# Kernel optimization log

Measured on AMD Instinct MI355X. Metric: run time of the kernel, lower is better.

The kernel has to match this reference:

```python
import jax, jax.numpy as jnp
import numpy as np

N_NODES = 100000
N_EDGES = 1600000
FEAT = 128
HID = 128
CLS = 4


def setup_inputs() -> dict:
    key = jax.random.key(0)
    ks = jax.random.split(key, 10)
    x = jax.random.normal(ks[0], (N_NODES, FEAT), dtype=jnp.float32)
    edge_index = jax.random.randint(ks[1], (2, N_EDGES), 0, N_NODES, dtype=jnp.int64)
    s1 = 1.0 / np.sqrt(FEAT)
    s2 = 1.0 / np.sqrt(HID)
    s3 = 1.0 / np.sqrt(CLS)
    return {
        "x": x,
        "edge_index": edge_index,
        "W1l": jax.random.uniform(ks[2], (HID, FEAT), jnp.float32, -s1, s1),
        "b1": jax.random.uniform(ks[3], (HID,), jnp.float32, -s1, s1),
        "W1r": jax.random.uniform(ks[4], (HID, FEAT), jnp.float32, -s1, s1),
        "W2l": jax.random.uniform(ks[5], (CLS, HID), jnp.float32, -s2, s2),
        "b2": jax.random.uniform(ks[6], (CLS,), jnp.float32, -s2, s2),
        "W2r": jax.random.uniform(ks[7], (CLS, HID), jnp.float32, -s2, s2),
        "Wlin": jax.random.uniform(ks[8], (2, CLS), jnp.float32, -s3, s3),
        "blin": jax.random.uniform(ks[9], (2,), jnp.float32, -s3, s3),
    }


def _sage_conv(h, src, dst, Wl, bl, Wr, n_nodes):
    # PyG SAGEConv (mean aggr, root_weight=True): lin_l(mean_j h_j) + lin_r(h_i)
    msg = h[src]  # [E, d] irregular gather
    agg = jax.ops.segment_sum(msg, dst, num_segments=n_nodes)  # [N, d]
    deg = jax.ops.segment_sum(jnp.ones((src.shape[0], 1), h.dtype), dst,
                              num_segments=n_nodes)  # [N, 1]
    agg = agg / jnp.maximum(deg, 1.0)
    return agg @ Wl.T + bl + h @ Wr.T


def reference(x, edge_index, W1l, b1, W1r, W2l, b2, W2r, Wlin, blin):
    n = x.shape[0]
    src, dst = edge_index[0], edge_index[1]
    h = jax.nn.relu(_sage_conv(x, src, dst, W1l, b1, W1r, n))
    # dropout is identity in eval mode (training=False)
    h = _sage_conv(h, src, dst, W2l, b2, W2r, n)  # [N, 4]
    return h @ Wlin.T + blin  # [N, 2]
```

## Files before the change

### kernel.cpp

```cpp
#include <hip/hip_runtime.h>

#define NN 100000
#define NE 1600000
#define NBUK 1563
#define EB 8192

typedef __attribute__((ext_vector_type(8))) short v8s;
typedef __attribute__((ext_vector_type(4))) float v4f;

__device__ __forceinline__ unsigned short f2bf(float f) {
  unsigned int u = __float_as_uint(f);
  unsigned int r = (u + 0x7FFFu + ((u >> 16) & 1u)) >> 16;
  return (unsigned short)r;
}
__device__ __forceinline__ float bflo(unsigned int w) { return __uint_as_float(w << 16); }
__device__ __forceinline__ float bfhi(unsigned int w) { return __uint_as_float(w & 0xFFFF0000u); }
__device__ __forceinline__ float bf2f(unsigned short w) {
  return __uint_as_float((unsigned int)w << 16);
}


__global__ void k_zerob(int* __restrict__ hist) {
  int i = blockIdx.x * blockDim.x + threadIdx.x;
  if (i < NBUK) hist[i] = 0;
}

__global__ __launch_bounds__(256) void k_hist(const int* __restrict__ dst,
                                              int* __restrict__ hist) {
  __shared__ int lh[NBUK];
  int t = threadIdx.x;
  for (int i = t; i < NBUK; i += 256) lh[i] = 0;
  __syncthreads();
  int base = blockIdx.x * 16384;
  int lim = min(16384, NE - base);
  for (int j = t; j < lim; j += 256) atomicAdd(&lh[dst[base + j] >> 6], 1);
  __syncthreads();
  for (int i = t; i < NBUK; i += 256) {
    int c = lh[i];
    if (c) atomicAdd(&hist[i], c);
  }
}

__global__ __launch_bounds__(256) void k_scanb(const int* __restrict__ hist,
                                               int* __restrict__ bbase,
                                               int* __restrict__ gcur) {
  __shared__ int sc[256];
  __shared__ int carry;
  int t = threadIdx.x;
  if (t == 0) carry = 0;
  __syncthreads();
  for (int c = 0; c < (NBUK + 255) / 256; ++c) {
    int i = c * 256 + t;
    int vv = (i < NBUK) ? hist[i] : 0;
    sc[t] = vv;
    __syncthreads();
    for (int o = 1; o < 256; o <<= 1) {
      int uu = (t >= o) ? sc[t - o] : 0;
      __syncthreads();
      sc[t] += uu;
      __syncthreads();
    }
    int excl = carry + sc[t] - vv;
    if (i < NBUK) { bbase[i] = excl; gcur[i] = excl; }
    __syncthreads();
    if (t == 0) carry += sc[255];
    __syncthreads();
  }
}

extern __shared__ char smem_dyn[];
__global__ __launch_bounds__(256) void k_scatter(const int* __restrict__ src,
                                                 const int* __restrict__ dst,
                                                 int* __restrict__ gcur,
                                                 unsigned int* __restrict__ staged) {
  unsigned int* stageP = (unsigned int*)smem_dyn;
  unsigned short* stageB = (unsigned short*)(stageP + EB);
  int* lhist  = (int*)(stageB + EB);
  int* lbase  = lhist + NBUK;
  int* lcur   = lbase + NBUK;
  int* gclaim = lcur + NBUK;
  __shared__ int sc[256];
  __shared__ int carry;
  int t = threadIdx.x;
  int e0 = blockIdx.x * EB;
  int ecnt = min(EB, NE - e0);
  for (int i = t; i < NBUK; i += 256) lhist[i] = 0;
  if (t == 0) carry = 0;
  __syncthreads();
  for (int j = t; j < ecnt; j += 256) atomicAdd(&lhist[dst[e0 + j] >> 6], 1);
  __syncthreads();
  for (int c = 0; c < (NBUK + 255) / 256; ++c) {
    int i = c * 256 + t;
    int vv = (i < NBUK) ? lhist[i] : 0;
    sc[t] = vv;
    __syncthreads();
    for (int o = 1; o < 256; o <<= 1) {
      int uu = (t >= o) ? sc[t - o] : 0;
      __syncthreads();
      sc[t] += uu;
      __syncthreads();
    }
    int excl = carry + sc[t] - vv;
    if (i < NBUK) { lbase[i] = excl; lcur[i] = excl; }
    __syncthreads();
    if (t == 0) carry += sc[255];
    __syncthreads();
  }
  for (int b = t; b < NBUK; b += 256) {
    int c = lhist[b];
    gclaim[b] = c ? atomicAdd(&gcur[b], c) : 0;
  }
  __syncthreads();
  for (int j = t; j < ecnt; j += 256) {
    int s = src[e0 + j], d = dst[e0 + j];
    int b = d >> 6;
    int lp = atomicAdd(&lcur[b], 1);
    stageP[lp] = ((unsigned int)s << 6) | (unsigned int)(d & 63);
    stageB[lp] = (unsigned short)b;
  }
  __syncthreads();
  for (int i = t; i < ecnt; i += 256) {
    int b = stageB[i];
    staged[gclaim[b] + (i - lbase[b])] = stageP[i];
  }
}

__global__ __launch_bounds__(256) void k_sort2(const unsigned int* __restrict__ staged,
                                               const int* __restrict__ bbase,
                                               const int* __restrict__ hist,
                                               int* __restrict__ csr,
                                               int* __restrict__ off,
                                               int* __restrict__ deg) {
  __shared__ int h64[64], c64[64];
  int bkt = blockIdx.x, t = threadIdx.x;
  if (t < 64) h64[t] = 0;
  __syncthreads();
  int st = bbase[bkt], cnt = hist[bkt];
  for (int j = t; j < cnt; j += 256) atomicAdd(&h64[staged[st + j] & 63], 1);
  __syncthreads();
  if (t < 64) {
    int v = h64[t];
    int inc = v;
    for (int o = 1; o < 64; o <<= 1) {
      int uu = __shfl_up(inc, o, 64);
      if (t >= o) inc += uu;
    }
    int excl = inc - v;
    c64[t] = excl;
    int node = bkt * 64 + t;
    if (node < NN) { off[node] = st + excl; deg[node] = v; }
  }
  __syncthreads();
  for (int j = t; j < cnt; j += 256) {
    unsigned pk = staged[st + j];
    int lp = atomicAdd(&c64[pk & 63], 1);
    csr[st + lp] = (int)(pk >> 6);
  }
}


__global__ void k_packw(const float* __restrict__ W1l, const float* __restrict__ W1r,
                        unsigned short* __restrict__ Wcat) {
  int i = blockIdx.x * blockDim.x + threadIdx.x;
  float f = (i < 16384) ? W1l[i] : W1r[i - 16384];
  Wcat[i] = f2bf(f);
}

__global__ __launch_bounds__(256) void k_gemm1(
    const float* __restrict__ x, const unsigned short* __restrict__ Wcat,
    unsigned short* __restrict__ u, unsigned short* __restrict__ v) {
  char* wlds = smem_dyn;
  int t = threadIdx.x;
  {
    int rsub = t >> 4, chunk = t & 15;
#pragma unroll
    for (int rd = 0; rd < 16; ++rd) {
      int row = rd * 16 + rsub;
      uint4 w4 = *(const uint4*)(Wcat + (size_t)row * 128 + chunk * 8);
      *(uint4*)(wlds + row * 272 + chunk * 16) = w4;
    }
  }

  int wave = t >> 6, l = t & 63;
  int m0 = blockIdx.x * 64 + wave * 16;
  int lr = l & 15, kq = l >> 4;
  int rowc = min(m0 + lr, NN - 1);

  v8s a[4];
#pragma unroll
  for (int ks = 0; ks < 4; ++ks) {
    const float* xp = x + (size_t)rowc * 128 + ks * 32 + kq * 8;
    float4 f0 = *(const float4*)xp;
    float4 f1 = *(const float4*)(xp + 4);
    v8s tv;
    tv[0] = (short)f2bf(f0.x); tv[1] = (short)f2bf(f0.y);
    tv[2] = (short)f2bf(f0.z); tv[3] = (short)f2bf(f0.w);
    tv[4] = (short)f2bf(f1.x); tv[5] = (short)f2bf(f1.y);
    tv[6] = (short)f2bf(f1.z); tv[7] = (short)f2bf(f1.w);
    a[ks] = tv;
  }

  __syncthreads();

  v4f acc[16];
#pragma unroll
  for (int nt = 0; nt < 16; ++nt) acc[nt] = (v4f){0.f, 0.f, 0.f, 0.f};

#pragma unroll
  for (int nt = 0; nt < 16; ++nt) {
    const char* wrow = wlds + (nt * 16 + lr) * 272;
#pragma unroll
    for (int ks = 0; ks < 4; ++ks) {
      v8s b = *(const v8s*)(wrow + ks * 64 + kq * 16);
      acc[nt] = __builtin_amdgcn_mfma_f32_16x16x32_bf16(b, a[ks], acc[nt], 0, 0, 0);
    }
  }

  if (m0 + lr < NN) {
    size_t rowb = (size_t)(m0 + lr) * 128;
#pragma unroll
    for (int nt = 0; nt < 16; ++nt) {
      unsigned lo = (unsigned)f2bf(acc[nt][0]) | ((unsigned)f2bf(acc[nt][1]) << 16);
      unsigned hi = (unsigned)f2bf(acc[nt][2]) | ((unsigned)f2bf(acc[nt][3]) << 16);
      int col = (nt & 7) * 16 + kq * 4;
      if (nt < 8) *(uint2*)(u + rowb + col) = make_uint2(lo, hi);
      else        *(uint2*)(v + rowb + col) = make_uint2(lo, hi);
    }
  }
}

__global__ __launch_bounds__(256) void k_agg(
    const unsigned short* __restrict__ u, const unsigned short* __restrict__ v,
    const int* __restrict__ csr, const int* __restrict__ off, const int* __restrict__ deg,
    const float* __restrict__ b1,
    const float* __restrict__ W2l, const float* __restrict__ W2r,
    float* __restrict__ p, float* __restrict__ r) {
  int wid = (blockIdx.x * blockDim.x + threadIdx.x) >> 6;
  int l = threadIdx.x & 63;
  if (wid >= NN) return;
  int cnt = deg[wid], st = off[wid];
  int half = l >> 5;
  int dpos = l & 31;
  const char* ubase = (const char*)u + (dpos << 3);

  uint2 vw = *(const uint2*)((const char*)v + ((size_t)wid << 8) + (dpos << 3));
  float4 bb = *(const float4*)(b1 + 4 * dpos);
  const float* Wbase = half ? W2r : W2l;
  float4 wv[4];
#pragma unroll
  for (int o = 0; o < 4; ++o) wv[o] = *(const float4*)(Wbase + o * 128 + 4 * dpos);

  float a0 = 0.f, a1 = 0.f, a2 = 0.f, a3 = 0.f;

#define LOADW(W, S) uint2 W = *(const uint2*)(ubase + ((size_t)((unsigned)(S) << 8)))
#define ACCW(W) { a0 += bflo(W.x); a1 += bfhi(W.x); a2 += bflo(W.y); a3 += bfhi(W.y); }

  for (int base = 0; base < cnt; base += 64) {
    int nloc = min(64, cnt - base);
    int idx = 0;
    if (l < nloc) idx = csr[st + base + l];
    int npair = nloc >> 1;
    int e = 0;
    for (; e + 8 <= npair; e += 8) {
      int s0 = __shfl(idx, 2 * e + half, 64);
      int s1 = __shfl(idx, 2 * (e + 1) + half, 64);
      int s2 = __shfl(idx, 2 * (e + 2) + half, 64);
      int s3 = __shfl(idx, 2 * (e + 3) + half, 64);
      int s4 = __shfl(idx, 2 * (e + 4) + half, 64);
      int s5 = __shfl(idx, 2 * (e + 5) + half, 64);
      int s6 = __shfl(idx, 2 * (e + 6) + half, 64);
      int s7 = __shfl(idx, 2 * (e + 7) + half, 64);
      LOADW(w0, s0);
      LOADW(w1, s1);
      LOADW(w2, s2);
      LOADW(w3, s3);
      LOADW(w4, s4);
      LOADW(w5, s5);
      LOADW(w6, s6);
      LOADW(w7, s7);
      ACCW(w0); ACCW(w1); ACCW(w2); ACCW(w3);
      ACCW(w4); ACCW(w5); ACCW(w6); ACCW(w7);
    }
    for (; e + 4 <= npair; e += 4) {
      int s0 = __shfl(idx, 2 * e + half, 64);
      int s1 = __shfl(idx, 2 * (e + 1) + half, 64);
      int s2 = __shfl(idx, 2 * (e + 2) + half, 64);
      int s3 = __shfl(idx, 2 * (e + 3) + half, 64);
      LOADW(w0, s0);
      LOADW(w1, s1);
      LOADW(w2, s2);
      LOADW(w3, s3);
      ACCW(w0); ACCW(w1); ACCW(w2); ACCW(w3);
    }
    for (; e < npair; ++e) {
      int s = __shfl(idx, 2 * e + half, 64);
      LOADW(w, s);
      ACCW(w);
    }
    if (nloc & 1) {
      int s = __shfl(idx, nloc - 1, 64);
      if (half == 0) {
        LOADW(w, s);
        ACCW(w);
      }
    }
  }
#undef LOADW
#undef ACCW

  a0 += __shfl_xor(a0, 32, 64);
  a1 += __shfl_xor(a1, 32, 64);
  a2 += __shfl_xor(a2, 32, 64);
  a3 += __shfl_xor(a3, 32, 64);

  float inv = 1.f / (float)max(cnt, 1);
  float h0 = fmaxf(fmaf(a0, inv, bflo(vw.x) + bb.x), 0.f);
  float h1 = fmaxf(fmaf(a1, inv, bfhi(vw.x) + bb.y), 0.f);
  float h2 = fmaxf(fmaf(a2, inv, bflo(vw.y) + bb.z), 0.f);
  float h3 = fmaxf(fmaf(a3, inv, bfhi(vw.y) + bb.w), 0.f);

  float t0 = h0 * wv[0].x + h1 * wv[0].y + h2 * wv[0].z + h3 * wv[0].w;
  float t1 = h0 * wv[1].x + h1 * wv[1].y + h2 * wv[1].z + h3 * wv[1].w;
  float t2 = h0 * wv[2].x + h1 * wv[2].y + h2 * wv[2].z + h3 * wv[2].w;
  float t3 = h0 * wv[3].x + h1 * wv[3].y + h2 * wv[3].z + h3 * wv[3].w;
  float v01 = (l & 1) ? t1 : t0;
  float w01 = __shfl_xor((l & 1) ? t0 : t1, 1, 64);
  float r01 = v01 + w01;
  float v23 = (l & 1) ? t3 : t2;
  float w23 = __shfl_xor((l & 1) ? t2 : t3, 1, 64);
  float r23 = v23 + w23;
  float vq = (l & 2) ? r23 : r01;
  float wq = __shfl_xor((l & 2) ? r01 : r23, 2, 64);
  float rr = vq + wq;
  rr += __shfl_xor(rr, 4, 64);
  rr += __shfl_xor(rr, 8, 64);
  rr += __shfl_xor(rr, 16, 64);
  float* outp = half ? r : p;
  if (dpos < 4) outp[(size_t)wid * 4 + dpos] = rr;
}

__global__ __launch_bounds__(256) void k_final(
    const float* __restrict__ p, const float* __restrict__ r,
    const int* __restrict__ csr, const int* __restrict__ off,
    const int* __restrict__ deg,
    const float* __restrict__ b2,
    const float* __restrict__ Wlin, const float* __restrict__ blin,
    float* __restrict__ out) {
  int gid = blockIdx.x * blockDim.x + threadIdx.x;
  int node = gid >> 3;
  int sl = gid & 7;
  if (node >= NN) return;
  int cnt = deg[node], st = off[node];
  int l = threadIdx.x & 63;

  float a0 = 0.f, a1 = 0.f, a2 = 0.f, a3 = 0.f;
  for (int e = sl; e < cnt; e += 8) {
    int s = csr[st + e];
    const float4 pv = *(const float4*)(p + (size_t)s * 4);
    a0 += pv.x; a1 += pv.y; a2 += pv.z; a3 += pv.w;
  }
  float v01 = (l & 1) ? a1 : a0;
  float w01 = __shfl_xor((l & 1) ? a0 : a1, 1, 64);
  float r01 = v01 + w01;
  float v23 = (l & 1) ? a3 : a2;
  float w23 = __shfl_xor((l & 1) ? a2 : a3, 1, 64);
  float r23 = v23 + w23;
  float vq = (l & 2) ? r23 : r01;
  float wq = __shfl_xor((l & 2) ? r01 : r23, 2, 64);
  float rr = vq + wq;
  rr += __shfl_xor(rr, 4, 64);
  int o = sl & 3;
  float inv = 1.f / (float)max(cnt, 1);
  float g = rr * inv + b2[o] + r[(size_t)node * 4 + o];
  float t0 = g * Wlin[o];
  float t1 = g * Wlin[4 + o];
  float vv = (l & 1) ? t1 : t0;
  float ww = __shfl_xor((l & 1) ? t0 : t1, 1, 64);
  float q = vv + ww;
  q += __shfl_xor(q, 2, 64);
  if (sl < 2) out[(size_t)node * 2 + sl] = q + blin[sl];
}


extern "C" void kernel_launch(void* const* d_in, const int* in_sizes, int n_in,
                              void* d_out, int out_size, void* d_ws, size_t ws_size,
                              hipStream_t stream) {
  const float* x    = (const float*)d_in[0];
  const int*   ei   = (const int*)d_in[1];
  const int*   src  = ei;
  const int*   dst  = ei + NE;
  const float* W1l  = (const float*)d_in[2];
  const float* b1   = (const float*)d_in[3];
  const float* W1r  = (const float*)d_in[4];
  const float* W2l  = (const float*)d_in[5];
  const float* b2   = (const float*)d_in[6];
  const float* W2r  = (const float*)d_in[7];
  const float* Wlin = (const float*)d_in[8];
  const float* blin = (const float*)d_in[9];
  float* out = (float*)d_out;

  char* w = (char*)d_ws;
  size_t o = 0;
  auto alloc = [&](size_t bytes) {
    void* pp = (void*)(w + o);
    o = (o + bytes + 255) & ~(size_t)255;
    return pp;
  };
  int* hist  = (int*)alloc(NBUK * 4);
  int* bbase = (int*)alloc(NBUK * 4);
  int* gcur  = (int*)alloc(NBUK * 4);
  unsigned int*  staged = (unsigned int*)alloc((size_t)NE * 4);
  int* csr   = (int*)alloc((size_t)NE * 4);
  int* offs  = (int*)alloc(NN * 4);
  int* deg   = (int*)alloc(NN * 4);
  unsigned short* Wcat  = (unsigned short*)alloc(256 * 128 * 2);
  unsigned short* ubuf  = (unsigned short*)alloc((size_t)NN * 128 * 2);
  unsigned short* vbuf  = (unsigned short*)alloc((size_t)NN * 128 * 2);
  float* pbuf = (float*)alloc((size_t)NN * 4 * 4);
  float* rbuf = (float*)alloc((size_t)NN * 4 * 4);

  const size_t scatter_lds = (size_t)EB * 4 + (size_t)EB * 2 + (size_t)4 * NBUK * 4;
  const size_t gemm1_lds = 256 * 272;

  hipLaunchKernelGGL(k_zerob, dim3((NBUK + 255) / 256), dim3(256), 0, stream, hist);
  hipLaunchKernelGGL(k_hist,  dim3((NE + 16383) / 16384), dim3(256), 0, stream, dst, hist);
  hipLaunchKernelGGL(k_scanb, dim3(1), dim3(256), 0, stream, hist, bbase, gcur);
  hipLaunchKernelGGL(k_scatter, dim3((NE + EB - 1) / EB), dim3(256), scatter_lds, stream,
                     src, dst, gcur, staged);
  hipLaunchKernelGGL(k_sort2, dim3(NBUK), dim3(256), 0, stream,
                     staged, bbase, hist, csr, offs, deg);
  hipLaunchKernelGGL(k_packw, dim3(128), dim3(256), 0, stream, W1l, W1r, Wcat);
  hipLaunchKernelGGL(k_gemm1, dim3((NN + 63) / 64), dim3(256), gemm1_lds, stream,
                     x, Wcat, ubuf, vbuf);
  hipLaunchKernelGGL(k_agg,   dim3((NN * 64 + 255) / 256), dim3(256), 0, stream,
                     ubuf, vbuf, csr, offs, deg, b1, W2l, W2r, pbuf, rbuf);
  hipLaunchKernelGGL(k_final, dim3((NN * 8 + 255) / 256), dim3(256), 0, stream,
                     pbuf, rbuf, csr, offs, deg, b2, Wlin, blin, out);
}
```

Measured before the change: 281.0 us.

## Simplify bucket scatter, use wave-shuffle scan, widen aggregation gathers

Three changes. The scatter kernel no longer does a local prefix scan and LDS staging; each edge is written directly to its globally claimed slot plus a per-bucket local counter. The single-block bucket scan now uses wave shuffles instead of barrier-heavy LDS steps. The layer-1 aggregation now has each lane gather 16 bytes (8 bf16 features), so four edges are in flight per wave step instead of two, with reductions and the output projection adjusted to match. Risks: the direct scatter writes are less coalesced than the staged copy, and there is more register pressure in the aggregation.

Measured after the change: 276.3 us. About the same (-1.7%).

```diff
diff --git a/kernel.cpp b/kernel.cpp
--- a/kernel.cpp
+++ b/kernel.cpp
@@ -44,68 +44,44 @@
 __global__ __launch_bounds__(256) void k_scanb(const int* __restrict__ hist,
                                                int* __restrict__ bbase,
                                                int* __restrict__ gcur) {
-  __shared__ int sc[256];
-  __shared__ int carry;
-  int t = threadIdx.x;
-  if (t == 0) carry = 0;
-  __syncthreads();
+  __shared__ int wsum[4];
+  int t = threadIdx.x, w = t >> 6, l = t & 63;
+  int carry = 0;
   for (int c = 0; c < (NBUK + 255) / 256; ++c) {
     int i = c * 256 + t;
     int vv = (i < NBUK) ? hist[i] : 0;
-    sc[t] = vv;
+    int inc = vv;
+#pragma unroll
+    for (int o = 1; o < 64; o <<= 1) {
+      int uu = __shfl_up(inc, o, 64);
+      if (l >= o) inc += uu;
+    }
+    if (l == 63) wsum[w] = inc;
     __syncthreads();
-    for (int o = 1; o < 256; o <<= 1) {
-      int uu = (t >= o) ? sc[t - o] : 0;
-      __syncthreads();
-      sc[t] += uu;
-      __syncthreads();
-    }
-    int excl = carry + sc[t] - vv;
+    int woff = 0;
+    for (int j = 0; j < w; ++j) woff += wsum[j];
+    int excl = carry + woff + inc - vv;
     if (i < NBUK) { bbase[i] = excl; gcur[i] = excl; }
+    int tot = wsum[0] + wsum[1] + wsum[2] + wsum[3];
     __syncthreads();
-    if (t == 0) carry += sc[255];
-    __syncthreads();
-  }
-}
-
-extern __shared__ char smem_dyn[];
+    carry += tot;
+  }
+}
+
 __global__ __launch_bounds__(256) void k_scatter(const int* __restrict__ src,
                                                  const int* __restrict__ dst,
                                                  int* __restrict__ gcur,
                                                  unsigned int* __restrict__ staged) {
-  unsigned int* stageP = (unsigned int*)smem_dyn;
-  unsigned short* stageB = (unsigned short*)(stageP + EB);
-  int* lhist  = (int*)(stageB + EB);
-  int* lbase  = lhist + NBUK;
-  int* lcur   = lbase + NBUK;
-  int* gclaim = lcur + NBUK;
-  __shared__ int sc[256];
-  __shared__ int carry;
+  __shared__ int lhist[NBUK];
+  __shared__ int lcur[NBUK];
+  __shared__ int gclaim[NBUK];
   int t = threadIdx.x;
   int e0 = blockIdx.x * EB;
   int ecnt = min(EB, NE - e0);
-  for (int i = t; i < NBUK; i += 256) lhist[i] = 0;
-  if (t == 0) carry = 0;
+  for (int i = t; i < NBUK; i += 256) { lhist[i] = 0; lcur[i] = 0; }
   __syncthreads();
   for (int j = t; j < ecnt; j += 256) atomicAdd(&lhist[dst[e0 + j] >> 6], 1);
   __syncthreads();
-  for (int c = 0; c < (NBUK + 255) / 256; ++c) {
-    int i = c * 256 + t;
-    int vv = (i < NBUK) ? lhist[i] : 0;
-    sc[t] = vv;
-    __syncthreads();
-    for (int o = 1; o < 256; o <<= 1) {
-      int uu = (t >= o) ? sc[t - o] : 0;
-      __syncthreads();
-      sc[t] += uu;
-      __syncthreads();
-    }
-    int excl = carry + sc[t] - vv;
-    if (i < NBUK) { lbase[i] = excl; lcur[i] = excl; }
-    __syncthreads();
-    if (t == 0) carry += sc[255];
-    __syncthreads();
-  }
   for (int b = t; b < NBUK; b += 256) {
     int c = lhist[b];
     gclaim[b] = c ? atomicAdd(&gcur[b], c) : 0;
@@ -115,13 +91,7 @@
     int s = src[e0 + j], d = dst[e0 + j];
     int b = d >> 6;
     int lp = atomicAdd(&lcur[b], 1);
-    stageP[lp] = ((unsigned int)s << 6) | (unsigned int)(d & 63);
-    stageB[lp] = (unsigned short)b;
-  }
-  __syncthreads();
-  for (int i = t; i < ecnt; i += 256) {
-    int b = stageB[i];
-    staged[gclaim[b] + (i - lbase[b])] = stageP[i];
+    staged[gclaim[b] + lp] = ((unsigned int)s << 6) | (unsigned int)(d & 63);
   }
 }
 
@@ -166,6 +136,7 @@
   Wcat[i] = f2bf(f);
 }
 
+extern __shared__ char smem_dyn[];
 __global__ __launch_bounds__(256) void k_gemm1(
     const float* __restrict__ x, const unsigned short* __restrict__ Wcat,
     unsigned short* __restrict__ u, unsigned short* __restrict__ v) {
@@ -239,104 +210,96 @@
   int l = threadIdx.x & 63;
   if (wid >= NN) return;
   int cnt = deg[wid], st = off[wid];
-  int half = l >> 5;
-  int dpos = l & 31;
-  const char* ubase = (const char*)u + (dpos << 3);
-
-  uint2 vw = *(const uint2*)((const char*)v + ((size_t)wid << 8) + (dpos << 3));
-  float4 bb = *(const float4*)(b1 + 4 * dpos);
-  const float* Wbase = half ? W2r : W2l;
-  float4 wv[4];
-#pragma unroll
-  for (int o = 0; o < 4; ++o) wv[o] = *(const float4*)(Wbase + o * 128 + 4 * dpos);
+  int quarter = l >> 4;
+  int dp = l & 15;
+  const char* ubase = (const char*)u + (dp << 4);
+
+  uint4 vw = *(const uint4*)((const char*)v + ((size_t)wid << 8) + (dp << 4));
+  float4 bbA = *(const float4*)(b1 + 8 * dp);
+  float4 bbB = *(const float4*)(b1 + 8 * dp + 4);
+  int obase = quarter * 2;
+  const float* WrowLo = (obase < 4) ? (W2l + obase * 128) : (W2r + (obase - 4) * 128);
+  const float* WrowHi = WrowLo + 128;
+  float4 wl0 = *(const float4*)(WrowLo + 8 * dp);
+  float4 wl1 = *(const float4*)(WrowLo + 8 * dp + 4);
+  float4 wh0 = *(const float4*)(WrowHi + 8 * dp);
+  float4 wh1 = *(const float4*)(WrowHi + 8 * dp + 4);
 
   float a0 = 0.f, a1 = 0.f, a2 = 0.f, a3 = 0.f;
-
-#define LOADW(W, S) uint2 W = *(const uint2*)(ubase + ((size_t)((unsigned)(S) << 8)))
-#define ACCW(W) { a0 += bflo(W.x); a1 += bfhi(W.x); a2 += bflo(W.y); a3 += bfhi(W.y); }
+  float a4 = 0.f, a5 = 0.f, a6 = 0.f, a7 = 0.f;
+
+#define LOADQ(W, S) uint4 W = *(const uint4*)(ubase + ((size_t)((unsigned)(S) << 8)))
+#define ACCQ(W) { a0 += bflo(W.x); a1 += bfhi(W.x); a2 += bflo(W.y); a3 += bfhi(W.y); \
+                  a4 += bflo(W.z); a5 += bfhi(W.z); a6 += bflo(W.w); a7 += bfhi(W.w); }
 
   for (int base = 0; base < cnt; base += 64) {
     int nloc = min(64, cnt - base);
     int idx = 0;
     if (l < nloc) idx = csr[st + base + l];
-    int npair = nloc >> 1;
+    int nquad = nloc >> 2;
     int e = 0;
-    for (; e + 8 <= npair; e += 8) {
-      int s0 = __shfl(idx, 2 * e + half, 64);
-      int s1 = __shfl(idx, 2 * (e + 1) + half, 64);
-      int s2 = __shfl(idx, 2 * (e + 2) + half, 64);
-      int s3 = __shfl(idx, 2 * (e + 3) + half, 64);
-      int s4 = __shfl(idx, 2 * (e + 4) + half, 64);
-      int s5 = __shfl(idx, 2 * (e + 5) + half, 64);
-      int s6 = __shfl(idx, 2 * (e + 6) + half, 64);
-      int s7 = __shfl(idx, 2 * (e + 7) + half, 64);
-      LOADW(w0, s0);
-      LOADW(w1, s1);
-      LOADW(w2, s2);
-      LOADW(w3, s3);
-      LOADW(w4, s4);
-      LOADW(w5, s5);
-      LOADW(w6, s6);
-      LOADW(w7, s7);
-      ACCW(w0); ACCW(w1); ACCW(w2); ACCW(w3);
-      ACCW(w4); ACCW(w5); ACCW(w6); ACCW(w7);
-    }
-    for (; e + 4 <= npair; e += 4) {
-      int s0 = __shfl(idx, 2 * e + half, 64);
-      int s1 = __shfl(idx, 2 * (e + 1) + half, 64);
-      int s2 = __shfl(idx, 2 * (e + 2) + half, 64);
-      int s3 = __shfl(idx, 2 * (e + 3) + half, 64);
-      LOADW(w0, s0);
-      LOADW(w1, s1);
-      LOADW(w2, s2);
-      LOADW(w3, s3);
-      ACCW(w0); ACCW(w1); ACCW(w2); ACCW(w3);
-    }
-    for (; e < npair; ++e) {
-      int s = __shfl(idx, 2 * e + half, 64);
-      LOADW(w, s);
-      ACCW(w);
-    }
-    if (nloc & 1) {
-      int s = __shfl(idx, nloc - 1, 64);
-      if (half == 0) {
-        LOADW(w, s);
-        ACCW(w);
+    for (; e + 4 <= nquad; e += 4) {
+      int s0 = __shfl(idx, 4 * e + quarter, 64);
+      int s1 = __shfl(idx, 4 * (e + 1) + quarter, 64);
+      int s2 = __shfl(idx, 4 * (e + 2) + quarter, 64);
+      int s3 = __shfl(idx, 4 * (e + 3) + quarter, 64);
+      LOADQ(w0, s0);
+      LOADQ(w1, s1);
+      LOADQ(w2, s2);
+      LOADQ(w3, s3);
+      ACCQ(w0); ACCQ(w1); ACCQ(w2); ACCQ(w3);
+    }
+    for (; e < nquad; ++e) {
+      int s = __shfl(idx, 4 * e + quarter, 64);
+      LOADQ(w, s);
+      ACCQ(w);
+    }
+    int rem = nloc & 3;
+    if (rem) {
+      int s = __shfl(idx, (nquad << 2) + quarter, 64);
+      if (quarter < rem) {
+        LOADQ(w, s);
+        ACCQ(w);
       }
     }
   }
-#undef LOADW
-#undef ACCW
-
-  a0 += __shfl_xor(a0, 32, 64);
-  a1 += __shfl_xor(a1, 32, 64);
-  a2 += __shfl_xor(a2, 32, 64);
-  a3 += __shfl_xor(a3, 32, 64);
+#undef LOADQ
+#undef ACCQ
+
+  a0 += __shfl_xor(a0, 16, 64); a0 += __shfl_xor(a0, 32, 64);
+  a1 += __shfl_xor(a1, 16, 64); a1 += __shfl_xor(a1, 32, 64);
+  a2 += __shfl_xor(a2, 16, 64); a2 += __shfl_xor(a2, 32, 64);
+  a3 += __shfl_xor(a3, 16, 64); a3 += __shfl_xor(a3, 32, 64);
+  a4 += __shfl_xor(a4, 16, 64); a4 += __shfl_xor(a4, 32, 64);
+  a5 += __shfl_xor(a5, 16, 64); a5 += __shfl_xor(a5, 32, 64);
+  a6 += __shfl_xor(a6, 16, 64); a6 += __shfl_xor(a6, 32, 64);
+  a7 += __shfl_xor(a7, 16, 64); a7 += __shfl_xor(a7, 32, 64);
 
   float inv = 1.f / (float)max(cnt, 1);
-  float h0 = fmaxf(fmaf(a0, inv, bflo(vw.x) + bb.x), 0.f);
-  float h1 = fmaxf(fmaf(a1, inv, bfhi(vw.x) + bb.y), 0.f);
-  float h2 = fmaxf(fmaf(a2, inv, bflo(vw.y) + bb.z), 0.f);
-  float h3 = fmaxf(fmaf(a3, inv, bfhi(vw.y) + bb.w), 0.f);
-
-  float t0 = h0 * wv[0].x + h1 * wv[0].y + h2 * wv[0].z + h3 * wv[0].w;
-  float t1 = h0 * wv[1].x + h1 * wv[1].y + h2 * wv[1].z + h3 * wv[1].w;
-  float t2 = h0 * wv[2].x + h1 * wv[2].y + h2 * wv[2].z + h3 * wv[2].w;
-  float t3 = h0 * wv[3].x + h1 * wv[3].y + h2 * wv[3].z + h3 * wv[3].w;
-  float v01 = (l & 1) ? t1 : t0;
-  float w01 = __shfl_xor((l & 1) ? t0 : t1, 1, 64);
-  float r01 = v01 + w01;
-  float v23 = (l & 1) ? t3 : t2;
-  float w23 = __shfl_xor((l & 1) ? t2 : t3, 1, 64);
-  float r23 = v23 + w23;
-  float vq = (l & 2) ? r23 : r01;
-  float wq = __shfl_xor((l & 2) ? r01 : r23, 2, 64);
-  float rr = vq + wq;
-  rr += __shfl_xor(rr, 4, 64);
-  rr += __shfl_xor(rr, 8, 64);
-  rr += __shfl_xor(rr, 16, 64);
-  float* outp = half ? r : p;
-  if (dpos < 4) outp[(size_t)wid * 4 + dpos] = rr;
+  float h0 = fmaxf(fmaf(a0, inv, bflo(vw.x) + bbA.x), 0.f);
+  float h1 = fmaxf(fmaf(a1, inv, bfhi(vw.x) + bbA.y), 0.f);
+  float h2 = fmaxf(fmaf(a2, inv, bflo(vw.y) + bbA.z), 0.f);
+  float h3 = fmaxf(fmaf(a3, inv, bfhi(vw.y) + bbA.w), 0.f);
+  float h4 = fmaxf(fmaf(a4, inv, bflo(vw.z) + bbB.x), 0.f);
+  float h5 = fmaxf(fmaf(a5, inv, bfhi(vw.z) + bbB.y), 0.f);
+  float h6 = fmaxf(fmaf(a6, inv, bflo(vw.w) + bbB.z), 0.f);
+  float h7 = fmaxf(fmaf(a7, inv, bfhi(vw.w) + bbB.w), 0.f);
+
+  float tlo = h0 * wl0.x + h1 * wl0.y + h2 * wl0.z + h3 * wl0.w +
+              h4 * wl1.x + h5 * wl1.y + h6 * wl1.z + h7 * wl1.w;
+  float thi = h0 * wh0.x + h1 * wh0.y + h2 * wh0.z + h3 * wh0.w +
+              h4 * wh1.x + h5 * wh1.y + h6 * wh1.z + h7 * wh1.w;
+  float vsel = (l & 1) ? thi : tlo;
+  float wsel = __shfl_xor((l & 1) ? tlo : thi, 1, 64);
+  float s = vsel + wsel;
+  s += __shfl_xor(s, 2, 64);
+  s += __shfl_xor(s, 4, 64);
+  s += __shfl_xor(s, 8, 64);
+  if (dp < 2) {
+    int oo = obase + (l & 1);
+    if (oo < 4) p[(size_t)wid * 4 + oo] = s;
+    else        r[(size_t)wid * 4 + (oo - 4)] = s;
+  }
 }
 
 __global__ __launch_bounds__(256) void k_final(
@@ -419,13 +382,12 @@
   float* pbuf = (float*)alloc((size_t)NN * 4 * 4);
   float* rbuf = (float*)alloc((size_t)NN * 4 * 4);
 
-  const size_t scatter_lds = (size_t)EB * 4 + (size_t)EB * 2 + (size_t)4 * NBUK * 4;
   const size_t gemm1_lds = 256 * 272;
 
   hipLaunchKernelGGL(k_zerob, dim3((NBUK + 255) / 256), dim3(256), 0, stream, hist);
   hipLaunchKernelGGL(k_hist,  dim3((NE + 16383) / 16384), dim3(256), 0, stream, dst, hist);
   hipLaunchKernelGGL(k_scanb, dim3(1), dim3(256), 0, stream, hist, bbase, gcur);
-  hipLaunchKernelGGL(k_scatter, dim3((NE + EB - 1) / EB), dim3(256), scatter_lds, stream,
+  hipLaunchKernelGGL(k_scatter, dim3((NE + EB - 1) / EB), dim3(256), 0, stream,
                      src, dst, gcur, staged);
   hipLaunchKernelGGL(k_sort2, dim3(NBUK), dim3(256), 0, stream,
                      staged, bbase, hist, csr, offs, deg);
```
